# Performance work log

Measured on AMD Instinct MI355X. Metric: run time of the kernel, lower is better.

The kernel has to match this reference:

```python
import jax, jax.numpy as jnp
import numpy as np

# GDN (gated delta-rule) linear attention, prefill path, single packed sequence,
# no initial conv/ssm state.
NUM_K_HEADS = 16
NUM_V_HEADS = 32
HEAD_K_DIM = 128
HEAD_V_DIM = 128
HIDDEN = 2048
CONV_K = 4
EPS = 1e-6
K_TOTAL = NUM_K_HEADS * HEAD_K_DIM
V_TOTAL = NUM_V_HEADS * HEAD_V_DIM
QKV_TOTAL = 2 * K_TOTAL + V_TOTAL


def setup_inputs() -> dict:
    key = jax.random.key(0)
    ks = jax.random.split(key, 9)
    T = 2048
    s = 0.02
    return {
        "hidden_states": jax.random.normal(ks[0], (T, HIDDEN), jnp.float32),
        "in_proj_qkv_weight": s * jax.random.normal(ks[1], (QKV_TOTAL, HIDDEN), jnp.float32),
        "in_proj_z_weight": s * jax.random.normal(ks[2], (V_TOTAL, HIDDEN), jnp.float32),
        "in_proj_a_weight": s * jax.random.normal(ks[3], (NUM_V_HEADS, HIDDEN), jnp.float32),
        "in_proj_b_weight": s * jax.random.normal(ks[4], (NUM_V_HEADS, HIDDEN), jnp.float32),
        "conv1d_weight": 0.1 * jax.random.normal(ks[5], (QKV_TOTAL, CONV_K), jnp.float32),
        "out_proj_weight": s * jax.random.normal(ks[6], (HIDDEN, V_TOTAL), jnp.float32),
        "norm_weight": jnp.ones((HEAD_V_DIM,), jnp.float32),
        "A_log": jnp.log(jnp.linspace(1.0, 8.0, NUM_V_HEADS, dtype=jnp.float32)),
        "dt_bias": 0.5 * jax.random.normal(ks[7], (NUM_V_HEADS,), jnp.float32),
    }


def _causal_conv1d_silu(x, w):
    # x: [T, C], w: [C, K] depthwise causal conv + SiLU
    T = x.shape[0]
    K = w.shape[1]
    xp = jnp.pad(x, ((K - 1, 0), (0, 0)))
    y = xp[0:T] * w[:, 0]
    for j in range(1, K):  # small fixed K
        y = y + xp[j:j + T] * w[:, j]
    return jax.nn.silu(y)


def _l2norm(x):
    return x / jnp.sqrt(jnp.sum(x * x, axis=-1, keepdims=True) + EPS)


def _gdn_recurrence(q, k, v, g, beta, scale):
    # q,k: [T,Hv,Dk] (l2-normed, repeated over GQA groups), v: [T,Hv,Dv]
    # g,beta: [T,Hv]. State S: [Hv,Dk,Dv]. Gated delta rule:
    #   S <- exp(g)*S ; S <- S + k^T beta (v - k S) ; o = scale * q S
    Hv, Dk = q.shape[1], q.shape[2]
    Dv = v.shape[2]

    def step(S, inp):
        q_t, k_t, v_t, g_t, b_t = inp
        S = S * jnp.exp(g_t)[:, None, None]
        pred = jnp.einsum('hk,hkv->hv', k_t, S)
        delta = b_t[:, None] * (v_t - pred)
        S = S + jnp.einsum('hk,hv->hkv', k_t, delta)
        o = jnp.einsum('hk,hkv->hv', q_t * scale, S)
        return S, o

    S0 = jnp.zeros((Hv, Dk, Dv), q.dtype)
    _, o = jax.lax.scan(step, S0, (q, k, v, g, beta))
    return o  # [T,Hv,Dv]


def reference(hidden_states, in_proj_qkv_weight, in_proj_z_weight, in_proj_a_weight,
              in_proj_b_weight, conv1d_weight, out_proj_weight, norm_weight, A_log, dt_bias):
    T = hidden_states.shape[0]
    mixed = hidden_states @ in_proj_qkv_weight.T            # [T, QKV_TOTAL]
    z = hidden_states @ in_proj_z_weight.T                  # [T, V_TOTAL]
    a = hidden_states @ in_proj_a_weight.T                  # [T, Hv]
    b = hidden_states @ in_proj_b_weight.T                  # [T, Hv]

    mixed = _causal_conv1d_silu(mixed, conv1d_weight)

    q, k, v = jnp.split(mixed, [K_TOTAL, 2 * K_TOTAL], axis=-1)
    q = q.reshape(T, NUM_K_HEADS, HEAD_K_DIM)
    k = k.reshape(T, NUM_K_HEADS, HEAD_K_DIM)
    v = v.reshape(T, NUM_V_HEADS, HEAD_V_DIM)

    # qk l2-norm in kernel, GQA repeat to v heads
    q = _l2norm(q)
    k = _l2norm(k)
    ratio = NUM_V_HEADS // NUM_K_HEADS
    q = jnp.repeat(q, ratio, axis=1)
    k = jnp.repeat(k, ratio, axis=1)

    # fused_gdn_gating: g = -exp(A_log) * softplus(a + dt_bias); beta = sigmoid(b)
    g = -jnp.exp(A_log) * jax.nn.softplus(a + dt_bias)      # [T,Hv]
    beta = jax.nn.sigmoid(b)                                # [T,Hv]

    o = _gdn_recurrence(q, k, v, g, beta, HEAD_K_DIM ** -0.5)  # [T,Hv,Dv]

    # gated RMSNorm: rmsnorm(o) * norm_weight * silu(z)
    o = o * jax.lax.rsqrt(jnp.mean(o * o, axis=-1, keepdims=True) + EPS) * norm_weight
    o = o * jax.nn.silu(z.reshape(T, NUM_V_HEADS, HEAD_V_DIM))

    return o.reshape(T, -1) @ out_proj_weight.T             # [T, HIDDEN]
```

## Files before the change

### kernel.cpp

```cpp
#include <hip/hip_runtime.h>
#include <math.h>

#define T_SEQ     2048
#define HIDDEN_D  2048
#define NUM_KH    16
#define NUM_VH    32
#define HEAD_DIM  128
#define K_TOTAL   2048
#define V_TOTAL   4096
#define QKV_TOTAL 8192
#define EPS_F     1e-6f
#define CC        32
#define NCHUNK    (T_SEQ / CC)
#define NV        16

typedef __attribute__((ext_vector_type(4))) float f32x4;
typedef __attribute__((ext_vector_type(8))) short s16x8;

__device__ __forceinline__ unsigned short f2bf(float f) {
    unsigned int u = __float_as_uint(f);
    u += 0x7FFFu + ((u >> 16) & 1u);
    return (unsigned short)(u >> 16);
}

__global__ __launch_bounds__(256) void cast_bf16_kernel(
    const float* __restrict__ src, unsigned short* __restrict__ dst, int n4)
{
    int idx = blockIdx.x * 256 + threadIdx.x;
    if (idx >= n4) return;
    float4 v = ((const float4*)src)[idx];
    ushort4 o;
    o.x = f2bf(v.x); o.y = f2bf(v.y); o.z = f2bf(v.z); o.w = f2bf(v.w);
    ((ushort4*)dst)[idx] = o;
}

__global__ __launch_bounds__(256) void gemm_bt_bf16(
    const unsigned short* __restrict__ A, const unsigned short* __restrict__ B,
    float* __restrict__ C, int M, int N, int K)
{
    __shared__ unsigned short As[128 * 64];
    __shared__ unsigned short Bs[128 * 64];
    const int tid  = threadIdx.x;
    const int wave = tid >> 6;
    const int lane = tid & 63;
    const int m0 = blockIdx.y * 128;
    const int n0 = blockIdx.x * 128;
    const int wm = (wave >> 1) * 64;
    const int wn = (wave & 1) * 64;

    f32x4 acc[4][4];
    f32x4 zero = {0.f, 0.f, 0.f, 0.f};
#pragma unroll
    for (int i = 0; i < 4; ++i)
#pragma unroll
        for (int j = 0; j < 4; ++j) acc[i][j] = zero;

    const int srow = lane >> 3;
    const int scol = (lane & 7) * 8;
    const int rm = lane & 15;
    const int koq = (lane >> 4) * 8;

    for (int kt = 0; kt < K; kt += 64) {
#pragma unroll
        for (int l = 0; l < 4; ++l) {
            const int r0 = wave * 32 + l * 8;
            const unsigned short* ga =
                A + (size_t)(m0 + r0 + srow) * K + kt + scol;
            const unsigned short* gb =
                B + (size_t)(n0 + r0 + srow) * K + kt + scol;
            __builtin_amdgcn_global_load_lds(
                (const __attribute__((address_space(1))) void*)ga,
                (__attribute__((address_space(3))) void*)&As[r0 * 64], 16, 0, 0);
            __builtin_amdgcn_global_load_lds(
                (const __attribute__((address_space(1))) void*)gb,
                (__attribute__((address_space(3))) void*)&Bs[r0 * 64], 16, 0, 0);
        }
        __syncthreads();

#pragma unroll
        for (int ks = 0; ks < 2; ++ks) {
            const int ko = ks * 32 + koq;
            s16x8 af[4], bfr[4];
#pragma unroll
            for (int i = 0; i < 4; ++i) {
                af[i]  = *(const s16x8*)&As[(wm + i * 16 + rm) * 64 + ko];
                bfr[i] = *(const s16x8*)&Bs[(wn + i * 16 + rm) * 64 + ko];
            }
#pragma unroll
            for (int i = 0; i < 4; ++i)
#pragma unroll
                for (int j = 0; j < 4; ++j)
                    acc[i][j] = __builtin_amdgcn_mfma_f32_16x16x32_bf16(
                        af[i], bfr[j], acc[i][j], 0, 0, 0);
        }
        __syncthreads();
    }

    const int cr = (lane >> 4) * 4;
    const int ccol = lane & 15;
#pragma unroll
    for (int i = 0; i < 4; ++i)
#pragma unroll
        for (int j = 0; j < 4; ++j) {
#pragma unroll
            for (int r = 0; r < 4; ++r)
                C[(size_t)(m0 + wm + i * 16 + cr + r) * N
                  + n0 + wn + j * 16 + ccol] = acc[i][j][r];
        }
}

__global__ __launch_bounds__(256) void gemm_nt_64(
    const float* __restrict__ A, const float* __restrict__ B,
    float* __restrict__ C, int M, int N, int K)
{
    __shared__ float As[16][68];
    __shared__ float Bs[16][68];
    const int tid = threadIdx.x;
    const int m0 = blockIdx.y * 64;
    const int n0 = blockIdx.x * 64;
    const int tm = tid >> 4;
    const int tn = tid & 15;
    const int lr = tid >> 2;
    const int lc = (tid & 3) * 4;

    float acc[4][4];
#pragma unroll
    for (int i = 0; i < 4; ++i)
#pragma unroll
        for (int j = 0; j < 4; ++j) acc[i][j] = 0.f;

    for (int kt = 0; kt < K; kt += 16) {
        float4 av = *(const float4*)(A + (size_t)(m0 + lr) * K + kt + lc);
        float4 bv = *(const float4*)(B + (size_t)(n0 + lr) * K + kt + lc);
        As[lc + 0][lr] = av.x; As[lc + 1][lr] = av.y;
        As[lc + 2][lr] = av.z; As[lc + 3][lr] = av.w;
        Bs[lc + 0][lr] = bv.x; Bs[lc + 1][lr] = bv.y;
        Bs[lc + 2][lr] = bv.z; Bs[lc + 3][lr] = bv.w;
        __syncthreads();
#pragma unroll
        for (int kk = 0; kk < 16; ++kk) {
            float4 a4 = *(const float4*)&As[kk][tm * 4];
            float4 b4 = *(const float4*)&Bs[kk][tn * 4];
            float a[4] = {a4.x, a4.y, a4.z, a4.w};
            float b[4] = {b4.x, b4.y, b4.z, b4.w};
#pragma unroll
            for (int i = 0; i < 4; ++i)
#pragma unroll
                for (int j = 0; j < 4; ++j)
                    acc[i][j] = fmaf(a[i], b[j], acc[i][j]);
        }
        __syncthreads();
    }
#pragma unroll
    for (int i = 0; i < 4; ++i) {
        float4 o = make_float4(acc[i][0], acc[i][1], acc[i][2], acc[i][3]);
        *(float4*)(C + (size_t)(m0 + tm * 4 + i) * N + n0 + tn * 4) = o;
    }
}

__global__ __launch_bounds__(256) void concat_ab_kernel(
    const float* __restrict__ Wa, const float* __restrict__ Wb,
    float* __restrict__ Wab)
{
    int idx = blockIdx.x * 256 + threadIdx.x;
    int half = 16384;
    const float* src = (idx < half) ? Wa : Wb;
    int off = (idx < half) ? idx : idx - half;
    ((float4*)Wab)[idx] = ((const float4*)src)[off];
}

__global__ __launch_bounds__(256) void gating_finalize_kernel(
    const float* __restrict__ ab, const float* __restrict__ A_log,
    const float* __restrict__ dt_bias, float* __restrict__ g,
    float* __restrict__ beta)
{
    int idx = blockIdx.x * 256 + threadIdx.x;
    int t = idx >> 5, h = idx & 31;
    float a = ab[t * 64 + h] + dt_bias[h];
    float b = ab[t * 64 + 32 + h];
    float sp = (a > 20.f) ? a : log1pf(expf(a));
    g[idx] = -expf(A_log[h]) * sp;
    beta[idx] = 1.f / (1.f + expf(-b));
}

__global__ __launch_bounds__(256) void conv_silu_kernel(
    const float* __restrict__ mixed, const float* __restrict__ cw,
    float* __restrict__ qkv)
{
    int idx = blockIdx.x * 256 + threadIdx.x;
    int c = idx & (QKV_TOTAL - 1);
    int t = idx >> 13;
    const float4 w = *(const float4*)(cw + (size_t)c * 4);
    float y = w.w * mixed[(size_t)t * QKV_TOTAL + c];
    if (t >= 1) y = fmaf(w.z, mixed[(size_t)(t - 1) * QKV_TOTAL + c], y);
    if (t >= 2) y = fmaf(w.y, mixed[(size_t)(t - 2) * QKV_TOTAL + c], y);
    if (t >= 3) y = fmaf(w.x, mixed[(size_t)(t - 3) * QKV_TOTAL + c], y);
    qkv[(size_t)t * QKV_TOTAL + c] = y / (1.f + expf(-y));
}

__global__ __launch_bounds__(64) void l2norm_kernel(float* __restrict__ qkv)
{
    const int row = blockIdx.x;
    const int t = row >> 5;
    const int r = row & 31;
    float* p = qkv + (size_t)t * QKV_TOTAL + r * HEAD_DIM;
    const int lane = threadIdx.x;
    float2 v = *(float2*)(p + lane * 2);
    float s = v.x * v.x + v.y * v.y;
    for (int off = 32; off > 0; off >>= 1) s += __shfl_down(s, off);
    s = __shfl(s, 0);
    float inv = rsqrtf(s + EPS_F);
    v.x *= inv; v.y *= inv;
    *(float2*)(p + lane * 2) = v;
}

__global__ __launch_bounds__(256) void gdn_p1(
    const float* __restrict__ qkv, const float* __restrict__ g,
    const float* __restrict__ beta, float* __restrict__ Tbuf,
    float* __restrict__ Pbuf, float* __restrict__ lam_g,
    float* __restrict__ bet_g, float* __restrict__ rl_g)
{
    __shared__ float Kn[CC][132];
    __shared__ float Qn[CC][132];
    __shared__ float Wm[CC][33];
    __shared__ float Tld[CC][34];
    __shared__ float cums[CC];
    __shared__ float betas[CC];

    const int tid = threadIdx.x;
    const int h   = blockIdx.x;
    const int cix = blockIdx.y;
    const int t0  = cix * CC;
    const int kh  = h >> 1;
    const float scale = 0.08838834764831845f;
    const size_t mb = ((size_t)cix * NUM_VH + h);
    const size_t sb = mb * CC;

    if (tid < CC) {
        float x = g[(size_t)(t0 + tid) * NUM_VH + h];
        float bv = beta[(size_t)(t0 + tid) * NUM_VH + h];
#pragma unroll
        for (int off = 1; off < 32; off <<= 1) {
            float n = __shfl_up(x, off);
            if (tid >= off) x += n;
        }
        cums[tid] = x;
        betas[tid] = bv;
        float c31 = __shfl(x, 31);
        lam_g[sb + tid] = expf(x);
        bet_g[sb + tid] = bv;
        rl_g[sb + tid]  = expf(c31 - x);
    }
#pragma unroll
    for (int p = 0; p < 4; ++p) {
        int idx = p * 256 + tid;
        int i = idx >> 5, k4 = (idx & 31) * 4;
        const float* qr = qkv + (size_t)(t0 + i) * QKV_TOTAL + kh * HEAD_DIM + k4;
        float4 q4 = *(const float4*)qr;
        float4 k4v = *(const float4*)(qr + K_TOTAL);
        *(float4*)&Kn[i][k4] = k4v;
        q4.x *= scale; q4.y *= scale; q4.z *= scale; q4.w *= scale;
        *(float4*)&Qn[i][k4] = q4;
    }
    __syncthreads();

    {
        const int i0 = (tid >> 4) * 2, j0 = (tid & 15) * 2;
        float wa[2][2] = {{0.f, 0.f}, {0.f, 0.f}};
        float pa[2][2] = {{0.f, 0.f}, {0.f, 0.f}};
        for (int k = 0; k < HEAD_DIM; k += 4) {
            float4 a0 = *(const float4*)&Kn[i0][k];
            float4 a1 = *(const float4*)&Kn[i0 + 1][k];
            float4 b0 = *(const float4*)&Kn[j0][k];
            float4 b1 = *(const float4*)&Kn[j0 + 1][k];
            float4 c0 = *(const float4*)&Qn[i0][k];
            float4 c1 = *(const float4*)&Qn[i0 + 1][k];
            const float* ap0 = (const float*)&a0;
            const float* ap1 = (const float*)&a1;
            const float* bp0 = (const float*)&b0;
            const float* bp1 = (const float*)&b1;
            const float* cp0 = (const float*)&c0;
            const float* cp1 = (const float*)&c1;
#pragma unroll
            for (int cc = 0; cc < 4; ++cc) {
                wa[0][0] = fmaf(ap0[cc], bp0[cc], wa[0][0]);
                wa[0][1] = fmaf(ap0[cc], bp1[cc], wa[0][1]);
                wa[1][0] = fmaf(ap1[cc], bp0[cc], wa[1][0]);
                wa[1][1] = fmaf(ap1[cc], bp1[cc], wa[1][1]);
                pa[0][0] = fmaf(cp0[cc], bp0[cc], pa[0][0]);
                pa[0][1] = fmaf(cp0[cc], bp1[cc], pa[0][1]);
                pa[1][0] = fmaf(cp1[cc], bp0[cc], pa[1][0]);
                pa[1][1] = fmaf(cp1[cc], bp1[cc], pa[1][1]);
            }
        }
        float* Pg = Pbuf + mb * (CC * CC);
#pragma unroll
        for (int di = 0; di < 2; ++di)
#pragma unroll
            for (int dj = 0; dj < 2; ++dj) {
                int i = i0 + di, j = j0 + dj;
                float rr = expf(fminf(cums[i] - cums[j], 0.f));
                Wm[i][j] = (j < i) ? betas[i] * rr * wa[di][dj] : 0.f;
                Pg[i * CC + j] = (j <= i) ? rr * pa[di][dj] : 0.f;
            }
    }
    __syncthreads();

    {
        const int col = tid >> 3, tk = tid & 7;
        if (tk == 0) Tld[0][col] = (col == 0) ? 1.f : 0.f;
        for (int i = 1; i < CC; ++i) {
            float part = 0.f;
            for (int j = tk; j < i; j += 8)
                part = fmaf(Wm[i][j], Tld[j][col], part);
            part += __shfl_xor(part, 4);
            part += __shfl_xor(part, 2);
            part += __shfl_xor(part, 1);
            if (tk == 0) Tld[i][col] = ((i == col) ? 1.f : 0.f) - part;
        }
    }
    __syncthreads();
    {
        const int i = tid >> 3, j0 = (tid & 7) * 4;
        float4 t4 = make_float4(Tld[i][j0], Tld[i][j0 + 1],
                                Tld[i][j0 + 2], Tld[i][j0 + 3]);
        *(float4*)(Tbuf + mb * (CC * CC) + tid * 4) = t4;
    }
}

__global__ __launch_bounds__(256) void gdn_p2(
    const float* __restrict__ qkv, const float* __restrict__ Tbuf,
    const float* __restrict__ Pbuf, const float* __restrict__ lam_g,
    const float* __restrict__ bet_g, const float* __restrict__ rl_g,
    float* __restrict__ o)
{
    __shared__ float Kn[CC][132];
    __shared__ float Qn[CC][132];
    __shared__ float Sm[HEAD_DIM][NV + 2];
    __shared__ float Tm[CC][34];
    __shared__ float Pm[CC][34];
    __shared__ float Dl[CC][NV + 2];
    __shared__ float D2[CC][NV + 2];
    __shared__ float lamS[CC], betS[CC], rlS[CC];

    const int tid = threadIdx.x;
    const int h   = blockIdx.x >> 3;
    const int V0  = (blockIdx.x & 7) * NV;
    const int kh  = h >> 1;
    const float scale = 0.08838834764831845f;

    const int ri = tid >> 3;
    const int rn = (tid & 7) * 2;
    const int fk = (tid >> 3) * 4;

#pragma unroll
    for (int c = 0; c < 4; ++c) {
        Sm[fk + c][rn] = 0.f;
        Sm[fk + c][rn + 1] = 0.f;
    }

    for (int cix = 0; cix < NCHUNK; ++cix) {
        const int t0 = cix * CC;
        const size_t mb = ((size_t)cix * NUM_VH + h);
        __syncthreads();

#pragma unroll
        for (int p = 0; p < 4; ++p) {
            int idx = p * 256 + tid;
            int i = idx >> 5, k4 = (idx & 31) * 4;
            const float* qr = qkv + (size_t)(t0 + i) * QKV_TOTAL + kh * HEAD_DIM + k4;
            float4 q4 = *(const float4*)qr;
            float4 k4v = *(const float4*)(qr + K_TOTAL);
            *(float4*)&Kn[i][k4] = k4v;
            q4.x *= scale; q4.y *= scale; q4.z *= scale; q4.w *= scale;
            *(float4*)&Qn[i][k4] = q4;
        }
        {
            float4 t4 = *(const float4*)(Tbuf + mb * (CC * CC) + tid * 4);
            float4 p4 = *(const float4*)(Pbuf + mb * (CC * CC) + tid * 4);
            const int i = tid >> 3, j0 = (tid & 7) * 4;
            Tm[i][j0] = t4.x; Tm[i][j0 + 1] = t4.y;
            Tm[i][j0 + 2] = t4.z; Tm[i][j0 + 3] = t4.w;
            Pm[i][j0] = p4.x; Pm[i][j0 + 1] = p4.y;
            Pm[i][j0 + 2] = p4.z; Pm[i][j0 + 3] = p4.w;
        }
        if (tid < CC) {
            lamS[tid] = lam_g[mb * CC + tid];
            betS[tid] = bet_g[mb * CC + tid];
            rlS[tid]  = rl_g[mb * CC + tid];
        }
        float2 v2 = *(const float2*)(qkv + (size_t)(t0 + ri) * QKV_TOTAL
                                     + 2 * K_TOTAL + h * HEAD_DIM + V0 + rn);
        __syncthreads();

        float r1x = 0.f, r1y = 0.f, r2x = 0.f, r2y = 0.f;
        for (int k = 0; k < HEAD_DIM; k += 4) {
            float4 kv = *(const float4*)&Kn[ri][k];
            float4 qv = *(const float4*)&Qn[ri][k];
            const float* kp = (const float*)&kv;
            const float* qp = (const float*)&qv;
#pragma unroll
            for (int c4 = 0; c4 < 4; ++c4) {
                float2 s = *(const float2*)&Sm[k + c4][rn];
                r1x = fmaf(kp[c4], s.x, r1x);
                r1y = fmaf(kp[c4], s.y, r1y);
                r2x = fmaf(qp[c4], s.x, r2x);
                r2y = fmaf(qp[c4], s.y, r2y);
            }
        }
        float lam = lamS[ri], bet = betS[ri];
        Dl[ri][rn]     = bet * (v2.x - lam * r1x);
        Dl[ri][rn + 1] = bet * (v2.y - lam * r1y);
        float o1x = lam * r2x, o1y = lam * r2y;
        __syncthreads();

        {
            float dx = 0.f, dy = 0.f;
            for (int j = 0; j < CC; ++j) {
                float t = Tm[ri][j];
                float2 d = *(const float2*)&Dl[j][rn];
                dx = fmaf(t, d.x, dx);
                dy = fmaf(t, d.y, dy);
            }
            D2[ri][rn] = dx; D2[ri][rn + 1] = dy;
        }
        __syncthreads();

        {
            float ox = o1x, oy = o1y;
            for (int j = 0; j < CC; ++j) {
                float p = Pm[ri][j];
                float2 d = *(const float2*)&D2[j][rn];
                ox = fmaf(p, d.x, ox);
                oy = fmaf(p, d.y, oy);
            }
            *(float2*)(o + (size_t)(t0 + ri) * V_TOTAL + h * HEAD_DIM + V0 + rn)
                = make_float2(ox, oy);
        }

        {
            const float lamL = lamS[CC - 1];
            float s[4][2];
#pragma unroll
            for (int c = 0; c < 4; ++c) {
                s[c][0] = lamL * Sm[fk + c][rn];
                s[c][1] = lamL * Sm[fk + c][rn + 1];
            }
            for (int j = 0; j < CC; ++j) {
                float rl = rlS[j];
                float4 kj = *(const float4*)&Kn[j][fk];
                float2 dj = *(const float2*)&D2[j][rn];
                float rdx = rl * dj.x, rdy = rl * dj.y;
                const float* kp = (const float*)&kj;
#pragma unroll
                for (int c = 0; c < 4; ++c) {
                    s[c][0] = fmaf(kp[c], rdx, s[c][0]);
                    s[c][1] = fmaf(kp[c], rdy, s[c][1]);
                }
            }
#pragma unroll
            for (int c = 0; c < 4; ++c) {
                Sm[fk + c][rn] = s[c][0];
                Sm[fk + c][rn + 1] = s[c][1];
            }
        }
    }
}

__global__ __launch_bounds__(64) void rmsnorm_gate_kernel(
    float* __restrict__ o, const float* __restrict__ z,
    const float* __restrict__ nw)
{
    const int row = blockIdx.x;
    float* p = o + (size_t)row * HEAD_DIM;
    const float* zp = z + (size_t)row * HEAD_DIM;
    const int lane = threadIdx.x;
    float2 v = *(float2*)(p + lane * 2);
    float s = v.x * v.x + v.y * v.y;
    for (int off = 32; off > 0; off >>= 1) s += __shfl_down(s, off);
    s = __shfl(s, 0);
    float inv = rsqrtf(s * (1.f / HEAD_DIM) + EPS_F);
    float2 zv = *(float2*)(zp + lane * 2);
    float2 wv = *(const float2*)(nw + lane * 2);
    v.x = v.x * inv * wv.x * (zv.x / (1.f + expf(-zv.x)));
    v.y = v.y * inv * wv.y * (zv.y / (1.f + expf(-zv.y)));
    *(float2*)(p + lane * 2) = v;
}

extern "C" void kernel_launch(void* const* d_in, const int* in_sizes, int n_in,
                              void* d_out, int out_size, void* d_ws,
                              size_t ws_size, hipStream_t stream)
{
    const float* hs    = (const float*)d_in[0];
    const float* Wqkv  = (const float*)d_in[1];
    const float* Wz    = (const float*)d_in[2];
    const float* Wa    = (const float*)d_in[3];
    const float* Wb    = (const float*)d_in[4];
    const float* cw    = (const float*)d_in[5];
    const float* Wout  = (const float*)d_in[6];
    const float* nw    = (const float*)d_in[7];
    const float* A_log = (const float*)d_in[8];
    const float* dtb   = (const float*)d_in[9];
    float* out = (float*)d_out;

    float* F     = (float*)d_ws;
    float* mixed = F;
    float* qkvb  = F + (size_t)16777216;
    float* zb    = F + (size_t)33554432;
    float* gb    = F + (size_t)41943040;
    float* bb    = F + (size_t)42008576;
    float* ob    = mixed;

    float* Tbuf  = F + (size_t)8388608;
    float* Pbuf  = F + (size_t)10485760;
    float* lam_b = F + (size_t)12582912;
    float* bet_b = F + (size_t)12648448;
    float* rl_b  = F + (size_t)12713984;

    unsigned short* hs_bf   = (unsigned short*)(F + (size_t)16777216);
    unsigned short* Wqkv_bf = (unsigned short*)(F + (size_t)18874368);
    unsigned short* Wz_bf   = (unsigned short*)(F + (size_t)27262976);
    unsigned short* ob_bf   = (unsigned short*)(F + (size_t)33554432);
    unsigned short* Wout_bf = (unsigned short*)(F + (size_t)37748736);

    float* Wab = F + (size_t)27262976;
    float* ab  = F + (size_t)27394048;

    cast_bf16_kernel<<<1048576 / 256, 256, 0, stream>>>(hs, hs_bf, 1048576);
    cast_bf16_kernel<<<4194304 / 256, 256, 0, stream>>>(Wqkv, Wqkv_bf, 4194304);
    cast_bf16_kernel<<<2097152 / 256, 256, 0, stream>>>(Wz, Wz_bf, 2097152);
    gemm_bt_bf16<<<dim3(QKV_TOTAL / 128, T_SEQ / 128), 256, 0, stream>>>(
        hs_bf, Wqkv_bf, mixed, T_SEQ, QKV_TOTAL, HIDDEN_D);
    gemm_bt_bf16<<<dim3(V_TOTAL / 128, T_SEQ / 128), 256, 0, stream>>>(
        hs_bf, Wz_bf, zb, T_SEQ, V_TOTAL, HIDDEN_D);
    concat_ab_kernel<<<32768 / 256, 256, 0, stream>>>(Wa, Wb, Wab);
    gemm_nt_64<<<dim3(1, T_SEQ / 64), 256, 0, stream>>>(
        hs, Wab, ab, T_SEQ, 64, HIDDEN_D);
    gating_finalize_kernel<<<(T_SEQ * NUM_VH) / 256, 256, 0, stream>>>(
        ab, A_log, dtb, gb, bb);
    conv_silu_kernel<<<(T_SEQ * QKV_TOTAL) / 256, 256, 0, stream>>>(
        mixed, cw, qkvb);
    l2norm_kernel<<<T_SEQ * 32, 64, 0, stream>>>(qkvb);
    gdn_p1<<<dim3(NUM_VH, NCHUNK), 256, 0, stream>>>(
        qkvb, gb, bb, Tbuf, Pbuf, lam_b, bet_b, rl_b);
    gdn_p2<<<NUM_VH * (HEAD_DIM / NV), 256, 0, stream>>>(
        qkvb, Tbuf, Pbuf, lam_b, bet_b, rl_b, ob);
    rmsnorm_gate_kernel<<<T_SEQ * NUM_VH, 64, 0, stream>>>(ob, zb, nw);
    cast_bf16_kernel<<<2097152 / 256, 256, 0, stream>>>(ob, ob_bf, 2097152);
    cast_bf16_kernel<<<2097152 / 256, 256, 0, stream>>>(Wout, Wout_bf, 2097152);
    gemm_bt_bf16<<<dim3(HIDDEN_D / 128, T_SEQ / 128), 256, 0, stream>>>(
        ob_bf, Wout_bf, out, T_SEQ, HIDDEN_D, V_TOTAL);
}
```

Before: 975.1 us.

## Precompute P·T and T-scaled keys in phase 1, halve V tile in recurrence

Phase 1 now folds the decay-weighted T matrix into the P matrix (PT = P·T) and precomputes rl-scaled K^T T products, stored as bf16, so phase 2 skips the separate D2 = T·D step and one barrier per chunk. Phase 2 splits the value dimension into 8-wide tiles, giving twice as many blocks, and splits the K reduction across two lanes with a shuffle. This shortens the sequential per-chunk chain in the recurrence kernel. In exchange it adds bf16 rounding to the state update and moves extra matmul work into the parallel phase 1.

```diff
diff --git a/kernel.cpp b/kernel.cpp
--- a/kernel.cpp
+++ b/kernel.cpp
@@ -12,15 +12,20 @@
 #define EPS_F     1e-6f
 #define CC        32
 #define NCHUNK    (T_SEQ / CC)
-#define NV        16
+#define NV        8
 
 typedef __attribute__((ext_vector_type(4))) float f32x4;
 typedef __attribute__((ext_vector_type(8))) short s16x8;
+typedef __attribute__((ext_vector_type(8))) unsigned short u16x8;
 
 __device__ __forceinline__ unsigned short f2bf(float f) {
     unsigned int u = __float_as_uint(f);
     u += 0x7FFFu + ((u >> 16) & 1u);
     return (unsigned short)(u >> 16);
+}
+
+__device__ __forceinline__ float bf2f(unsigned short h) {
+    return __uint_as_float((unsigned int)h << 16);
 }
 
 __global__ __launch_bounds__(256) void cast_bf16_kernel(
@@ -216,16 +221,19 @@
 
 __global__ __launch_bounds__(256) void gdn_p1(
     const float* __restrict__ qkv, const float* __restrict__ g,
-    const float* __restrict__ beta, float* __restrict__ Tbuf,
-    float* __restrict__ Pbuf, float* __restrict__ lam_g,
-    float* __restrict__ bet_g, float* __restrict__ rl_g)
+    const float* __restrict__ beta, float* __restrict__ PTbuf,
+    unsigned short* __restrict__ K2buf, float* __restrict__ lam_g,
+    float* __restrict__ bet_g)
 {
     __shared__ float Kn[CC][132];
     __shared__ float Qn[CC][132];
     __shared__ float Wm[CC][33];
-    __shared__ float Tld[CC][34];
+    __shared__ float Tld[CC][36];
+    __shared__ float Pm[CC][33];
+    __shared__ float Trl[CC][33];
     __shared__ float cums[CC];
     __shared__ float betas[CC];
+    __shared__ float rlS[CC];
 
     const int tid = threadIdx.x;
     const int h   = blockIdx.x;
@@ -249,7 +257,7 @@
         float c31 = __shfl(x, 31);
         lam_g[sb + tid] = expf(x);
         bet_g[sb + tid] = bv;
-        rl_g[sb + tid]  = expf(c31 - x);
+        rlS[tid] = expf(c31 - x);
     }
 #pragma unroll
     for (int p = 0; p < 4; ++p) {
@@ -293,7 +301,6 @@
                 pa[1][1] = fmaf(cp1[cc], bp1[cc], pa[1][1]);
             }
         }
-        float* Pg = Pbuf + mb * (CC * CC);
 #pragma unroll
         for (int di = 0; di < 2; ++di)
 #pragma unroll
@@ -301,7 +308,7 @@
                 int i = i0 + di, j = j0 + dj;
                 float rr = expf(fminf(cums[i] - cums[j], 0.f));
                 Wm[i][j] = (j < i) ? betas[i] * rr * wa[di][dj] : 0.f;
-                Pg[i * CC + j] = (j <= i) ? rr * pa[di][dj] : 0.f;
+                Pm[i][j] = (j <= i) ? rr * pa[di][dj] : 0.f;
             }
     }
     __syncthreads();
@@ -320,44 +327,86 @@
         }
     }
     __syncthreads();
+
     {
         const int i = tid >> 3, j0 = (tid & 7) * 4;
-        float4 t4 = make_float4(Tld[i][j0], Tld[i][j0 + 1],
-                                Tld[i][j0 + 2], Tld[i][j0 + 3]);
-        *(float4*)(Tbuf + mb * (CC * CC) + tid * 4) = t4;
+        const float r = rlS[i];
+#pragma unroll
+        for (int e = 0; e < 4; ++e)
+            Trl[i][j0 + e] = Tld[i][j0 + e] * r;
+        float4 accp = {0.f, 0.f, 0.f, 0.f};
+        for (int m = 0; m < CC; ++m) {
+            float pv = Pm[i][m];
+            float4 tv = *(const float4*)&Tld[m][j0];
+            accp.x = fmaf(pv, tv.x, accp.x);
+            accp.y = fmaf(pv, tv.y, accp.y);
+            accp.z = fmaf(pv, tv.z, accp.z);
+            accp.w = fmaf(pv, tv.w, accp.w);
+        }
+        *(float4*)(PTbuf + mb * (CC * CC) + tid * 4) = accp;
+    }
+    __syncthreads();
+
+    {
+        const int m0 = tid >> 3;
+        const int q  = (tid & 7) * 4;
+        float acc[4][4];
+#pragma unroll
+        for (int c = 0; c < 4; ++c)
+#pragma unroll
+            for (int e = 0; e < 4; ++e) acc[c][e] = 0.f;
+        for (int j = 0; j < CC; ++j) {
+            float t = Trl[j][m0];
+#pragma unroll
+            for (int c = 0; c < 4; ++c) {
+                float4 a = *(const float4*)&Kn[j][q + 32 * c];
+                acc[c][0] = fmaf(t, a.x, acc[c][0]);
+                acc[c][1] = fmaf(t, a.y, acc[c][1]);
+                acc[c][2] = fmaf(t, a.z, acc[c][2]);
+                acc[c][3] = fmaf(t, a.w, acc[c][3]);
+            }
+        }
+        unsigned short* kout =
+            K2buf + mb * (CC * HEAD_DIM) + m0 * HEAD_DIM + q;
+#pragma unroll
+        for (int c = 0; c < 4; ++c) {
+            ushort4 o4;
+            o4.x = f2bf(acc[c][0]); o4.y = f2bf(acc[c][1]);
+            o4.z = f2bf(acc[c][2]); o4.w = f2bf(acc[c][3]);
+            *(ushort4*)(kout + 32 * c) = o4;
+        }
     }
 }
 
 __global__ __launch_bounds__(256) void gdn_p2(
-    const float* __restrict__ qkv, const float* __restrict__ Tbuf,
-    const float* __restrict__ Pbuf, const float* __restrict__ lam_g,
-    const float* __restrict__ bet_g, const float* __restrict__ rl_g,
-    float* __restrict__ o)
+    const float* __restrict__ qkv, const float* __restrict__ PTbuf,
+    const unsigned short* __restrict__ K2buf, const float* __restrict__ lam_g,
+    const float* __restrict__ bet_g, float* __restrict__ o)
 {
     __shared__ float Kn[CC][132];
     __shared__ float Qn[CC][132];
+    __shared__ unsigned short K2l[CC][136];
+    __shared__ float PTl[CC][36];
     __shared__ float Sm[HEAD_DIM][NV + 2];
-    __shared__ float Tm[CC][34];
-    __shared__ float Pm[CC][34];
     __shared__ float Dl[CC][NV + 2];
-    __shared__ float D2[CC][NV + 2];
-    __shared__ float lamS[CC], betS[CC], rlS[CC];
+    __shared__ float lamS[CC], betS[CC];
 
     const int tid = threadIdx.x;
-    const int h   = blockIdx.x >> 3;
-    const int V0  = (blockIdx.x & 7) * NV;
+    const int h   = blockIdx.x >> 4;
+    const int V0  = (blockIdx.x & 15) * NV;
     const int kh  = h >> 1;
     const float scale = 0.08838834764831845f;
 
     const int ri = tid >> 3;
-    const int rn = (tid & 7) * 2;
+    const int rn = (tid & 3) * 2;
+    const int hh = (tid >> 2) & 1;
+    const int kb = hh * 64;
+
     const int fk = (tid >> 3) * 4;
-
-#pragma unroll
-    for (int c = 0; c < 4; ++c) {
-        Sm[fk + c][rn] = 0.f;
-        Sm[fk + c][rn + 1] = 0.f;
-    }
+    const int sn = tid & 7;
+
+#pragma unroll
+    for (int c = 0; c < 4; ++c) Sm[fk + c][sn] = 0.f;
 
     for (int cix = 0; cix < NCHUNK; ++cix) {
         const int t0 = cix * CC;
@@ -375,94 +424,84 @@
             q4.x *= scale; q4.y *= scale; q4.z *= scale; q4.w *= scale;
             *(float4*)&Qn[i][k4] = q4;
         }
+#pragma unroll
+        for (int p = 0; p < 2; ++p) {
+            int idx = p * 256 + tid;
+            int i = idx >> 4, k8 = (idx & 15) * 8;
+            *(u16x8*)&K2l[i][k8] =
+                *(const u16x8*)(K2buf + mb * (CC * HEAD_DIM) + i * HEAD_DIM + k8);
+        }
         {
-            float4 t4 = *(const float4*)(Tbuf + mb * (CC * CC) + tid * 4);
-            float4 p4 = *(const float4*)(Pbuf + mb * (CC * CC) + tid * 4);
-            const int i = tid >> 3, j0 = (tid & 7) * 4;
-            Tm[i][j0] = t4.x; Tm[i][j0 + 1] = t4.y;
-            Tm[i][j0 + 2] = t4.z; Tm[i][j0 + 3] = t4.w;
-            Pm[i][j0] = p4.x; Pm[i][j0 + 1] = p4.y;
-            Pm[i][j0 + 2] = p4.z; Pm[i][j0 + 3] = p4.w;
+            float4 t4 = *(const float4*)(PTbuf + mb * (CC * CC) + tid * 4);
+            *(float4*)&PTl[tid >> 3][(tid & 7) * 4] = t4;
         }
         if (tid < CC) {
             lamS[tid] = lam_g[mb * CC + tid];
             betS[tid] = bet_g[mb * CC + tid];
-            rlS[tid]  = rl_g[mb * CC + tid];
         }
         float2 v2 = *(const float2*)(qkv + (size_t)(t0 + ri) * QKV_TOTAL
                                      + 2 * K_TOTAL + h * HEAD_DIM + V0 + rn);
         __syncthreads();
 
         float r1x = 0.f, r1y = 0.f, r2x = 0.f, r2y = 0.f;
-        for (int k = 0; k < HEAD_DIM; k += 4) {
-            float4 kv = *(const float4*)&Kn[ri][k];
-            float4 qv = *(const float4*)&Qn[ri][k];
+        for (int k = 0; k < 64; k += 4) {
+            float4 kv = *(const float4*)&Kn[ri][kb + k];
+            float4 qv = *(const float4*)&Qn[ri][kb + k];
             const float* kp = (const float*)&kv;
             const float* qp = (const float*)&qv;
 #pragma unroll
             for (int c4 = 0; c4 < 4; ++c4) {
-                float2 s = *(const float2*)&Sm[k + c4][rn];
+                float2 s = *(const float2*)&Sm[kb + k + c4][rn];
                 r1x = fmaf(kp[c4], s.x, r1x);
                 r1y = fmaf(kp[c4], s.y, r1y);
                 r2x = fmaf(qp[c4], s.x, r2x);
                 r2y = fmaf(qp[c4], s.y, r2y);
             }
         }
-        float lam = lamS[ri], bet = betS[ri];
-        Dl[ri][rn]     = bet * (v2.x - lam * r1x);
-        Dl[ri][rn + 1] = bet * (v2.y - lam * r1y);
-        float o1x = lam * r2x, o1y = lam * r2y;
-        __syncthreads();
-
+        r1x += __shfl_xor(r1x, 4);
+        r1y += __shfl_xor(r1y, 4);
+        r2x += __shfl_xor(r2x, 4);
+        r2y += __shfl_xor(r2y, 4);
         {
-            float dx = 0.f, dy = 0.f;
+            float lam = lamS[ri], bet = betS[ri];
+            float dlx = bet * (v2.x - lam * r1x);
+            float dly = bet * (v2.y - lam * r1y);
+            r2x *= lam; r2y *= lam;
+            if (hh == 0) { Dl[ri][rn] = dlx; Dl[ri][rn + 1] = dly; }
+        }
+        __syncthreads();
+
+        {
+            float ox = r2x, oy = r2y;
             for (int j = 0; j < CC; ++j) {
-                float t = Tm[ri][j];
+                float p = PTl[ri][j];
                 float2 d = *(const float2*)&Dl[j][rn];
-                dx = fmaf(t, d.x, dx);
-                dy = fmaf(t, d.y, dy);
-            }
-            D2[ri][rn] = dx; D2[ri][rn + 1] = dy;
-        }
-        __syncthreads();
-
-        {
-            float ox = o1x, oy = o1y;
-            for (int j = 0; j < CC; ++j) {
-                float p = Pm[ri][j];
-                float2 d = *(const float2*)&D2[j][rn];
                 ox = fmaf(p, d.x, ox);
                 oy = fmaf(p, d.y, oy);
             }
-            *(float2*)(o + (size_t)(t0 + ri) * V_TOTAL + h * HEAD_DIM + V0 + rn)
-                = make_float2(ox, oy);
+            if (hh == 0)
+                *(float2*)(o + (size_t)(t0 + ri) * V_TOTAL + h * HEAD_DIM + V0 + rn)
+                    = make_float2(ox, oy);
         }
 
         {
             const float lamL = lamS[CC - 1];
-            float s[4][2];
-#pragma unroll
-            for (int c = 0; c < 4; ++c) {
-                s[c][0] = lamL * Sm[fk + c][rn];
-                s[c][1] = lamL * Sm[fk + c][rn + 1];
-            }
+            float s0 = lamL * Sm[fk + 0][sn];
+            float s1 = lamL * Sm[fk + 1][sn];
+            float s2 = lamL * Sm[fk + 2][sn];
+            float s3 = lamL * Sm[fk + 3][sn];
             for (int j = 0; j < CC; ++j) {
-                float rl = rlS[j];
-                float4 kj = *(const float4*)&Kn[j][fk];
-                float2 dj = *(const float2*)&D2[j][rn];
-                float rdx = rl * dj.x, rdy = rl * dj.y;
-                const float* kp = (const float*)&kj;
-#pragma unroll
-                for (int c = 0; c < 4; ++c) {
-                    s[c][0] = fmaf(kp[c], rdx, s[c][0]);
-                    s[c][1] = fmaf(kp[c], rdy, s[c][1]);
-                }
-            }
-#pragma unroll
-            for (int c = 0; c < 4; ++c) {
-                Sm[fk + c][rn] = s[c][0];
-                Sm[fk + c][rn + 1] = s[c][1];
-            }
+                ushort4 kk = *(const ushort4*)&K2l[j][fk];
+                float d = Dl[j][sn];
+                s0 = fmaf(bf2f(kk.x), d, s0);
+                s1 = fmaf(bf2f(kk.y), d, s1);
+                s2 = fmaf(bf2f(kk.z), d, s2);
+                s3 = fmaf(bf2f(kk.w), d, s3);
+            }
+            Sm[fk + 0][sn] = s0;
+            Sm[fk + 1][sn] = s1;
+            Sm[fk + 2][sn] = s2;
+            Sm[fk + 3][sn] = s3;
         }
     }
 }
@@ -511,11 +550,10 @@
     float* bb    = F + (size_t)42008576;
     float* ob    = mixed;
 
-    float* Tbuf  = F + (size_t)8388608;
-    float* Pbuf  = F + (size_t)10485760;
-    float* lam_b = F + (size_t)12582912;
-    float* bet_b = F + (size_t)12648448;
-    float* rl_b  = F + (size_t)12713984;
+    float* PTbuf = F + (size_t)8388608;
+    unsigned short* K2buf = (unsigned short*)(F + (size_t)10485760);
+    float* lam_b = F + (size_t)14680064;
+    float* bet_b = F + (size_t)14745600;
 
     unsigned short* hs_bf   = (unsigned short*)(F + (size_t)16777216);
     unsigned short* Wqkv_bf = (unsigned short*)(F + (size_t)18874368);
@@ -542,9 +580,9 @@
         mixed, cw, qkvb);
     l2norm_kernel<<<T_SEQ * 32, 64, 0, stream>>>(qkvb);
     gdn_p1<<<dim3(NUM_VH, NCHUNK), 256, 0, stream>>>(
-        qkvb, gb, bb, Tbuf, Pbuf, lam_b, bet_b, rl_b);
+        qkvb, gb, bb, PTbuf, K2buf, lam_b, bet_b);
     gdn_p2<<<NUM_VH * (HEAD_DIM / NV), 256, 0, stream>>>(
-        qkvb, Tbuf, Pbuf, lam_b, bet_b, rl_b, ob);
+        qkvb, PTbuf, K2buf, lam_b, bet_b, ob);
     rmsnorm_gate_kernel<<<T_SEQ * NUM_VH, 64, 0, stream>>>(ob, zb, nw);
     cast_bf16_kernel<<<2097152 / 256, 256, 0, stream>>>(ob, ob_bf, 2097152);
     cast_bf16_kernel<<<2097152 / 256, 256, 0, stream>>>(Wout, Wout_bf, 2097152);
```

Result: slower. 1.031 ms (+5.8%).
